# Kernel tuning notes

Measured on AMD Instinct MI355X. Metric: run time of the kernel, lower is better.

## Reference

```python
import math
import jax, jax.numpy as jnp
import numpy as np

B, M, H, K, L = 8, 512, 512, 8, 1024  # batch, block, hidden, heads, span
D = H // K  # head_dim = 64; key/value length = M + L


def _skew(X):
    # shift every row one step right: [B', M, L] -> [B', M, M+L]
    Bp, Mm, Ll = X.shape
    X = jnp.pad(X, ((0, 0), (0, 0), (0, Mm + 1)))
    X = X.reshape(Bp, -1)[:, :-Mm]
    return X.reshape(Bp, Mm, Mm + Ll)


def _unskew(X):
    # reverse of _skew: [B', M, M+L] -> [B', M, L]
    Bp, Mm, Lt = X.shape
    Ll = Lt - Mm
    X = X.reshape(Bp, -1)
    X = jnp.pad(X, ((0, 0), (0, Mm)))
    X = X.reshape(Bp, Mm, Mm + Ll + 1)
    return X[:, :, :Ll]


def _heads(x):
    # [B, T, K*D] -> [B*K, T, D]
    b, t, _ = x.shape
    return x.reshape(b, t, K, D).transpose(0, 2, 1, 3).reshape(b * K, t, D)


def setup_inputs() -> dict:
    key0 = jax.random.key(0)
    ks = jax.random.split(key0, 8)
    s = 1.0 / math.sqrt(H)
    return {
        "query": jax.random.normal(ks[0], (B, M, H), jnp.float32),
        "key": jax.random.normal(ks[1], (B, M + L, H), jnp.float32),
        "value": jax.random.normal(ks[2], (B, M + L, H), jnp.float32),
        "key_pe": jax.random.normal(ks[3], (1, D, L), jnp.float32),
        "Wq": jax.random.normal(ks[4], (H, H), jnp.float32) * s,
        "Wk": jax.random.normal(ks[5], (H, H), jnp.float32) * s,
        "Wv": jax.random.normal(ks[6], (H, H), jnp.float32) * s,
        "Wo": jax.random.normal(ks[7], (H, H), jnp.float32) * s,
    }


def reference(query, key, value, key_pe, Wq, Wk, Wv, Wo):
    q = _heads(query @ Wq.T)   # [B*K, M, D]
    k = _heads(key @ Wk.T)     # [B*K, M+L, D]
    v = _heads(value @ Wv.T)   # [B*K, M+L, D]

    attn_cont = jnp.einsum('bmd,bnd->bmn', q, k)       # [B*K, M, M+L]
    attn_cont = _unskew(attn_cont)                      # [B*K, M, L]
    attn_pos = jnp.einsum('bmd,dl->bml', q, key_pe[0])  # [B*K, M, L]
    attn = jax.nn.softmax((attn_cont + attn_pos) / math.sqrt(D), axis=-1)

    attn_sk = _skew(attn)                               # [B*K, M, M+L]
    out = jnp.einsum('bmn,bnd->bmd', attn_sk, v)        # [B*K, M, D]
    out = out.reshape(B, K, M, D).transpose(0, 2, 1, 3).reshape(B, M, K * D)
    return out @ Wo.T
```

## Files before the change

kernel.cpp:

```cpp
#include <hip/hip_runtime.h>
#include <hip/hip_bf16.h>
#include <cstddef>
#include <math.h>


#define HDIM 512
#define MQ 512
#define NK 1536
#define LSPAN 1024
#define SHIFT 5.0f

typedef _Float16 f16_t;
typedef f16_t f16x8 __attribute__((ext_vector_type(8)));
typedef f16_t f16x4 __attribute__((ext_vector_type(4)));
typedef float f32x4 __attribute__((ext_vector_type(4)));

#define MFMA16F(a, b, c) __builtin_amdgcn_mfma_f32_16x16x32_f16((a), (b), (c), 0, 0, 0)

__device__ __forceinline__ void async_cp16(const void* g, void* l) {
  __builtin_amdgcn_global_load_lds((const __attribute__((address_space(1))) void*)g,
                                   (__attribute__((address_space(3))) void*)l, 16, 0, 0);
}

__global__ void prep_all(const float* __restrict__ q, const float* __restrict__ k,
                         const float* __restrict__ v,
                         const float* __restrict__ Wq, const float* __restrict__ Wk,
                         const float* __restrict__ Wv, const float* __restrict__ Wo,
                         const float* __restrict__ pe,
                         f16_t* __restrict__ q16, f16_t* __restrict__ k16,
                         f16_t* __restrict__ v16,
                         f16_t* __restrict__ wq, f16_t* __restrict__ wk,
                         f16_t* __restrict__ wv, f16_t* __restrict__ wo,
                         f16_t* __restrict__ pet) {
  int y = blockIdx.y;
  int i = blockIdx.x * 256 + threadIdx.x;
  if (y < 3) {
    const float* s = (y == 0) ? q : (y == 1) ? k : v;
    f16_t* d = (y == 0) ? q16 : (y == 1) ? k16 : v16;
    int n4 = (y == 0) ? 524288 : 1572864;
    if (i >= n4) return;
    float4 x = ((const float4*)s)[i];
    f16x4 o;
    o[0] = (f16_t)x.x; o[1] = (f16_t)x.y; o[2] = (f16_t)x.z; o[3] = (f16_t)x.w;
    ((f16x4*)d)[i] = o;
  } else {
    if (i < 262144) {
      int seg = i >> 16, j = i & 65535;
      const float* s = (seg == 0) ? Wq : (seg == 1) ? Wk : (seg == 2) ? Wv : Wo;
      f16_t* d = (seg == 0) ? wq : (seg == 1) ? wk : (seg == 2) ? wv : wo;
      float4 x = ((const float4*)s)[j];
      f16x4 o;
      o[0] = (f16_t)x.x; o[1] = (f16_t)x.y; o[2] = (f16_t)x.z; o[3] = (f16_t)x.w;
      ((f16x4*)d)[j] = o;
    } else if (i < 327680) {
      int j = i - 262144;
      pet[(j & 1023) * 64 + (j >> 10)] = (f16_t)pe[j];
    }
  }
}

__global__ __launch_bounds__(256) void gemm3(
    const f16_t* __restrict__ q16, const f16_t* __restrict__ k16, const f16_t* __restrict__ v16,
    const f16_t* __restrict__ wq, const f16_t* __restrict__ wk, const f16_t* __restrict__ wv,
    f16_t* __restrict__ qo, f16_t* __restrict__ ko, f16_t* __restrict__ vT) {
  __shared__ alignas(16) f16_t As[2][8192];
  __shared__ alignas(16) f16_t Bs[2][8192];

  const int bx = blockIdx.x;
  const f16_t *A, *Bm;
  f16_t* C;
  int row0, col0, ldc;
  if (bx < 128) {
    int t = bx;
    A = q16; Bm = wq; C = qo; ldc = HDIM;
    row0 = (t >> 2) * 128; col0 = (t & 3) * 128;
  } else if (bx < 512) {
    int t = bx - 128;
    A = k16; Bm = wk; C = ko; ldc = HDIM;
    row0 = (t >> 2) * 128; col0 = (t & 3) * 128;
  } else {
    int t = bx - 512;
    int b = t / 48, u = t % 48;
    A = wv; Bm = v16 + (size_t)b * NK * HDIM;
    C = vT + (size_t)b * 512 * NK; ldc = NK;
    row0 = (u / 12) * 128; col0 = (u % 12) * 128;
  }

  const int tid = threadIdx.x;
  const int lane = tid & 63, wave = tid >> 6;
  const int quad = lane >> 4, l16 = lane & 15;
  const int wr = (wave & 1) * 64, wc = (wave >> 1) * 64;
  const int rstage = tid >> 3, cstage = tid & 7;

#pragma unroll
  for (int i = 0; i < 4; ++i) {
    int r = i * 32 + rstage;
    int csw = cstage ^ (r & 7);
    async_cp16(A  + (size_t)(row0 + r) * HDIM + csw * 8, &As[0][i * 2048 + wave * 512]);
    async_cp16(Bm + (size_t)(col0 + r) * HDIM + csw * 8, &Bs[0][i * 2048 + wave * 512]);
  }

  f32x4 acc[4][4] = {};
  for (int it = 0; it < 8; ++it) {
    const int buf = it & 1;
    __syncthreads();
    if (it + 1 < 8) {
      int k0 = (it + 1) * 64;
#pragma unroll
      for (int i = 0; i < 4; ++i) {
        int r = i * 32 + rstage;
        int csw = cstage ^ (r & 7);
        async_cp16(A  + (size_t)(row0 + r) * HDIM + k0 + csw * 8,
                   &As[buf ^ 1][i * 2048 + wave * 512]);
        async_cp16(Bm + (size_t)(col0 + r) * HDIM + k0 + csw * 8,
                   &Bs[buf ^ 1][i * 2048 + wave * 512]);
      }
    }
#pragma unroll
    for (int ks = 0; ks < 2; ++ks) {
      f16x8 af[4], bf[4];
#pragma unroll
      for (int i = 0; i < 4; ++i) {
        int rA = wr + i * 16 + l16;
        af[i] = *(const f16x8*)&As[buf][rA * 64 + (((ks * 4 + quad) ^ (rA & 7)) * 8)];
        int rB = wc + i * 16 + l16;
        bf[i] = *(const f16x8*)&Bs[buf][rB * 64 + (((ks * 4 + quad) ^ (rB & 7)) * 8)];
      }
#pragma unroll
      for (int i = 0; i < 4; ++i)
#pragma unroll
        for (int n = 0; n < 4; ++n)
          acc[i][n] = MFMA16F(af[i], bf[n], acc[i][n]);
    }
  }
#pragma unroll
  for (int i = 0; i < 4; ++i)
#pragma unroll
    for (int n = 0; n < 4; ++n)
#pragma unroll
      for (int r = 0; r < 4; ++r)
        C[(size_t)(row0 + wr + i * 16 + quad * 4 + r) * ldc + col0 + wc + n * 16 + l16] =
            (f16_t)acc[i][n][r];
}

__global__ __launch_bounds__(256) void attn2(const f16_t* __restrict__ q,
                                             const f16_t* __restrict__ k,
                                             const f16_t* __restrict__ vT,
                                             const f16_t* __restrict__ pet,
                                             f16_t* __restrict__ Opart,
                                             float* __restrict__ Lpart) {
  __shared__ alignas(16) f16_t Ks[2][4096];
  __shared__ alignas(16) f16_t Vs[4096];
  __shared__ alignas(16) f16_t Tst[4][128][20];
  __shared__ alignas(16) f16_t Ps[4][16][72];

  const int m0 = blockIdx.x * 64;
  const int bh = blockIdx.y;
  const int b = bh >> 3, kh = bh & 7;
  const int z = blockIdx.z;
  const int j0 = z ? 9 : 0, j1 = z ? 16 : 8;
  const int tid = threadIdx.x;
  const int lane = tid & 63, wave = tid >> 6;
  const int quad = lane >> 4, l16 = lane & 15;
  const int sr = wave * 16;
  const int rstage = tid >> 3, cstage = tid & 7;

  f16_t (*Tw)[20] = Tst[wave];
  f16_t (*Pw)[72] = Ps[wave];

  f16x8 qa0, qa1;
  {
    const f16_t* qrow = q + (size_t)(b * MQ + m0 + sr + l16) * HDIM + kh * 64;
    qa0 = *(const f16x8*)(qrow + quad * 8);
    qa1 = *(const f16x8*)(qrow + 32 + quad * 8);
#pragma unroll
    for (int e = 0; e < 8; ++e) {
      qa0[e] = (f16_t)((float)qa0[e] * 0.125f);
      qa1[e] = (f16_t)((float)qa1[e] * 0.125f);
    }
  }

  f16x8 ones;
#pragma unroll
  for (int e = 0; e < 8; ++e) ones[e] = (f16_t)1.0f;

  f32x4 oacc[4] = {};
  f32x4 lacc = {};

  const f16_t* kbh = k + (size_t)b * NK * HDIM + kh * 64;
  const f16_t* vbh = vT + (size_t)(b * 512 + kh * 64) * NK;

  if (z) {
#pragma unroll
    for (int ch = 0; ch < 4; ++ch) {
      int l = 512 + ch * 16 + l16;
      f16x8 s0 = *(const f16x8*)(pet + (size_t)l * 64 + quad * 8);
      f16x8 s1 = *(const f16x8*)(pet + (size_t)l * 64 + 32 + quad * 8);
      f32x4 tt = {};
      tt = MFMA16F(qa0, s0, tt);
      tt = MFMA16F(qa1, s1, tt);
      int sb = l + sr + quad * 4;
#pragma unroll
      for (int r = 0; r < 4; ++r)
        Tw[(sb + r) & 127][quad * 4 + r] = (f16_t)tt[r];
    }
  }

#pragma unroll
  for (int i = 0; i < 2; ++i) {
    int r = i * 32 + rstage;
    int nsrc = m0 + j0 * 64 + r;
    int csw = cstage ^ (r & 7);
    async_cp16(kbh + (size_t)nsrc * HDIM + csw * 8, &Ks[0][i * 2048 + wave * 512]);
  }

  int buf = 0;
  for (int j = j0; j <= j1; ++j, buf ^= 1) {
    __syncthreads();

    f16x8 pb0[4], pb1[4];
    if (j < 16) {
#pragma unroll
      for (int ch = 0; ch < 4; ++ch) {
        int l = j * 64 + ch * 16 + l16;
        pb0[ch] = *(const f16x8*)(pet + (size_t)l * 64 + quad * 8);
        pb1[ch] = *(const f16x8*)(pet + (size_t)l * 64 + 32 + quad * 8);
      }
    }
    {
      int ncol0 = m0 + j * 64;
#pragma unroll
      for (int i = 0; i < 2; ++i) {
        int d = i * 32 + rstage;
        int csw = cstage ^ (d & 7);
        async_cp16(vbh + (size_t)d * NK + ncol0 + csw * 8, &Vs[i * 2048 + wave * 512]);
      }
#pragma unroll
      for (int i = 0; i < 2; ++i) {
        int r = i * 32 + rstage;
        int nsrc = m0 + (j + 1) * 64 + r;
        nsrc = (nsrc < NK) ? nsrc : (NK - 1);
        int csw = cstage ^ (r & 7);
        async_cp16(kbh + (size_t)nsrc * HDIM + csw * 8, &Ks[buf ^ 1][i * 2048 + wave * 512]);
      }
    }
    if (j < 16) {
      const int l0 = j * 64;
#pragma unroll
      for (int ch = 0; ch < 4; ++ch) {
        f32x4 tt = {};
        tt = MFMA16F(qa0, pb0[ch], tt);
        tt = MFMA16F(qa1, pb1[ch], tt);
        int sb = l0 + ch * 16 + l16 + sr + quad * 4;
#pragma unroll
        for (int r = 0; r < 4; ++r)
          Tw[(sb + r) & 127][quad * 4 + r] = (f16_t)tt[r];
      }
    }
    f32x4 sacc[4];
#pragma unroll
    for (int ch = 0; ch < 4; ++ch) {
      int n = ch * 16 + l16;
      const f16_t* kr = &Ks[buf][n * 64];
      f16x8 kb0 = *(const f16x8*)&kr[(quad ^ (n & 7)) * 8];
      f16x8 kb1 = *(const f16x8*)&kr[((quad + 4) ^ (n & 7)) * 8];
      f32x4 s = {};
      s = MFMA16F(qa0, kb0, s);
      s = MFMA16F(qa1, kb1, s);
      sacc[ch] = s;
    }
#pragma unroll
    for (int ch = 0; ch < 4; ++ch) {
      int scol = (j * 64 + ch * 16 + l16) & 127;
      f16x4 tq = *(const f16x4*)&Tw[scol][quad * 4];
#pragma unroll
      for (int r = 0; r < 4; ++r) {
        int il = quad * 4 + r;
        int l = j * 64 + ch * 16 + l16 - sr - il;
        float pe_ = __expf(sacc[ch][r] + (float)tq[r] - SHIFT);
        float pv = (l >= 0 && l < LSPAN) ? pe_ : 0.f;
        Pw[il][ch * 16 + l16] = (f16_t)pv;
      }
    }
    f16x8 pa0 = *(const f16x8*)&Pw[l16][quad * 8];
    f16x8 pa1 = *(const f16x8*)&Pw[l16][32 + quad * 8];
    __builtin_amdgcn_s_waitcnt(0x0F72);
#pragma unroll
    for (int dch = 0; dch < 4; ++dch) {
      int d = dch * 16 + l16;
      const f16_t* vr = &Vs[d * 64];
      f16x8 vb0 = *(const f16x8*)&vr[(quad ^ (d & 7)) * 8];
      f16x8 vb1 = *(const f16x8*)&vr[((quad + 4) ^ (d & 7)) * 8];
      oacc[dch] = MFMA16F(pa0, vb0, oacc[dch]);
      oacc[dch] = MFMA16F(pa1, vb1, oacc[dch]);
    }
    lacc = MFMA16F(pa0, ones, lacc);
    lacc = MFMA16F(pa1, ones, lacc);
  }

  f16_t* Op = Opart + (size_t)z * 2097152;
#pragma unroll
  for (int r = 0; r < 4; ++r) {
    float inv = 1.0f / lacc[r];
    int m = m0 + sr + quad * 4 + r;
#pragma unroll
    for (int dch = 0; dch < 4; ++dch)
      Op[(size_t)(b * MQ + m) * HDIM + kh * 64 + dch * 16 + l16] =
          (f16_t)(oacc[dch][r] * inv);
    if (l16 == 0)
      Lpart[z * 32768 + bh * MQ + m] = lacc[r];
  }
}

__global__ __launch_bounds__(256) void gemm_wo(const f16_t* __restrict__ O0,
                                               const f16_t* __restrict__ O1,
                                               const float* __restrict__ Lpart,
                                               const f16_t* __restrict__ Bw,
                                               float* __restrict__ C) {
  __shared__ alignas(16) f16_t As[2][128][72];
  __shared__ alignas(16) f16_t Bs[2][4096];
  const int bx = blockIdx.x;
  const int row0 = (bx >> 3) * 128, col0 = (bx & 7) * 64;
  const int tid = threadIdx.x;
  const int lane = tid & 63, wave = tid >> 6;
  const int quad = lane >> 4, l16 = lane & 15;
  const int wr = (wave & 1) * 64, wc = (wave >> 1) * 32;
  const int rstage = tid >> 3, cstage = tid & 7;
  const int cA8 = (tid & 7) * 8;

  f16x8 areg[4];
  auto loadA = [&](int it) {
    int k0 = it * 64;
    int head = (k0 + cA8) >> 6;
#pragma unroll
    for (int i = 0; i < 4; ++i) {
      int rg = row0 + i * 32 + rstage;
      int li = ((rg >> 9) * 8 + head) * MQ + (rg & 511);
      float l0 = Lpart[li], l1 = Lpart[32768 + li];
      float w0 = l0 / (l0 + l1), w1 = 1.0f - w0;
      f16x8 o0 = *(const f16x8*)(O0 + (size_t)rg * HDIM + k0 + cA8);
      f16x8 o1 = *(const f16x8*)(O1 + (size_t)rg * HDIM + k0 + cA8);
      f16x8 a8;
#pragma unroll
      for (int e = 0; e < 8; ++e)
        a8[e] = (f16_t)((float)o0[e] * w0 + (float)o1[e] * w1);
      areg[i] = a8;
    }
  };

  loadA(0);
#pragma unroll
  for (int i = 0; i < 2; ++i) {
    int r = i * 32 + rstage;
    int csw = cstage ^ (r & 7);
    async_cp16(Bw + (size_t)(col0 + r) * HDIM + csw * 8, &Bs[0][i * 2048 + wave * 512]);
  }
#pragma unroll
  for (int i = 0; i < 4; ++i)
    *(f16x8*)&As[0][i * 32 + rstage][cA8] = areg[i];

  f32x4 acc[4][2] = {};
  for (int it = 0; it < 8; ++it) {
    const int buf = it & 1;
    __syncthreads();
    if (it + 1 < 8) {
      int k0 = (it + 1) * 64;
#pragma unroll
      for (int i = 0; i < 2; ++i) {
        int r = i * 32 + rstage;
        int csw = cstage ^ (r & 7);
        async_cp16(Bw + (size_t)(col0 + r) * HDIM + k0 + csw * 8,
                   &Bs[buf ^ 1][i * 2048 + wave * 512]);
      }
      loadA(it + 1);
    }
#pragma unroll
    for (int ks = 0; ks < 2; ++ks) {
      f16x8 af[4], bf[2];
#pragma unroll
      for (int i = 0; i < 4; ++i)
        af[i] = *(const f16x8*)&As[buf][wr + i * 16 + l16][(ks * 4 + quad) * 8];
#pragma unroll
      for (int n = 0; n < 2; ++n) {
        int rB = wc + n * 16 + l16;
        bf[n] = *(const f16x8*)&Bs[buf][rB * 64 + (((ks * 4 + quad) ^ (rB & 7)) * 8)];
      }
#pragma unroll
      for (int i = 0; i < 4; ++i)
#pragma unroll
        for (int n = 0; n < 2; ++n)
          acc[i][n] = MFMA16F(af[i], bf[n], acc[i][n]);
    }
    if (it + 1 < 8) {
#pragma unroll
      for (int i = 0; i < 4; ++i)
        *(f16x8*)&As[buf ^ 1][i * 32 + rstage][cA8] = areg[i];
    }
  }
#pragma unroll
  for (int i = 0; i < 4; ++i)
#pragma unroll
    for (int n = 0; n < 2; ++n)
#pragma unroll
      for (int r = 0; r < 4; ++r)
        C[(size_t)(row0 + wr + i * 16 + quad * 4 + r) * HDIM + col0 + wc + n * 16 + l16] =
            acc[i][n][r];
}

extern "C" void kernel_launch(void* const* d_in, const int* in_sizes, int n_in,
                              void* d_out, int out_size, void* d_ws, size_t ws_size,
                              hipStream_t stream) {
  const float* query  = (const float*)d_in[0];
  const float* key    = (const float*)d_in[1];
  const float* value  = (const float*)d_in[2];
  const float* key_pe = (const float*)d_in[3];
  const float* Wq     = (const float*)d_in[4];
  const float* Wk     = (const float*)d_in[5];
  const float* Wv     = (const float*)d_in[6];
  const float* Wo     = (const float*)d_in[7];
  float* out = (float*)d_out;

  f16_t* ws = (f16_t*)d_ws;
  f16_t* q16a = ws;
  f16_t* k16a = q16a + 2097152;
  f16_t* v16a = k16a + 6291456;
  f16_t* wq16 = v16a + 6291456;
  f16_t* wk16 = wq16 + 262144;
  f16_t* wv16 = wk16 + 262144;
  f16_t* wo16 = wv16 + 262144;
  f16_t* pet  = wo16 + 262144;
  f16_t* qo   = pet + 65536;
  f16_t* ko   = qo + 2097152;
  f16_t* vTo  = ko + 6291456;
  f16_t* Opart = k16a;
  float* Lpart = (float*)v16a;

  hipLaunchKernelGGL(prep_all, dim3(6144, 4), dim3(256), 0, stream,
                     query, key, value, Wq, Wk, Wv, Wo, key_pe,
                     q16a, k16a, v16a, wq16, wk16, wv16, wo16, pet);
  hipLaunchKernelGGL(gemm3, dim3(896), dim3(256), 0, stream,
                     q16a, k16a, v16a, wq16, wk16, wv16, qo, ko, vTo);
  hipLaunchKernelGGL(attn2, dim3(8, 64, 2), dim3(256), 0, stream,
                     qo, ko, vTo, pet, Opart, Lpart);
  hipLaunchKernelGGL(gemm_wo, dim3(256), dim3(256), 0, stream,
                     Opart, Opart + 2097152, Lpart, wo16, out);
}
```

Before: 210.2 us.

## Fold log2e into Q scale, use exp2, skip masking on interior tiles, add setprio

Folds log2(e)/sqrt(D) into the query prescale and the softmax shift into the stored positional term, so the inner loop uses exp2f directly without extra adds. The l-range masking is now applied only on the first and last tiles, since interior tiles never need it. The positional MFMA is moved after the QK MFMAs, s_setprio hints are placed around the MFMA sections, and the positional staging row pitch shrinks from 20 to 18 halves. Together these cut VALU work in the softmax step, at the cost of possible LDS bank conflicts from the new pitch and fp16 rounding of the shifted positional values.

```diff
diff --git a/kernel.cpp b/kernel.cpp
--- a/kernel.cpp
+++ b/kernel.cpp
@@ -8,7 +8,8 @@
 #define MQ 512
 #define NK 1536
 #define LSPAN 1024
-#define SHIFT 5.0f
+#define QSCALE 0.18033688f
+#define SHIFT2 7.2134752f
 
 typedef _Float16 f16_t;
 typedef f16_t f16x8 __attribute__((ext_vector_type(8)));
@@ -151,7 +152,7 @@
                                              float* __restrict__ Lpart) {
   __shared__ alignas(16) f16_t Ks[2][4096];
   __shared__ alignas(16) f16_t Vs[4096];
-  __shared__ alignas(16) f16_t Tst[4][128][20];
+  __shared__ alignas(16) f16_t Tst[4][128][18];
   __shared__ alignas(16) f16_t Ps[4][16][72];
 
   const int m0 = blockIdx.x * 64;
@@ -165,7 +166,7 @@
   const int sr = wave * 16;
   const int rstage = tid >> 3, cstage = tid & 7;
 
-  f16_t (*Tw)[20] = Tst[wave];
+  f16_t (*Tw)[18] = Tst[wave];
   f16_t (*Pw)[72] = Ps[wave];
 
   f16x8 qa0, qa1;
@@ -175,8 +176,8 @@
     qa1 = *(const f16x8*)(qrow + 32 + quad * 8);
 #pragma unroll
     for (int e = 0; e < 8; ++e) {
-      qa0[e] = (f16_t)((float)qa0[e] * 0.125f);
-      qa1[e] = (f16_t)((float)qa1[e] * 0.125f);
+      qa0[e] = (f16_t)((float)qa0[e] * QSCALE);
+      qa1[e] = (f16_t)((float)qa1[e] * QSCALE);
     }
   }
 
@@ -191,9 +192,10 @@
   const f16_t* vbh = vT + (size_t)(b * 512 + kh * 64) * NK;
 
   if (z) {
+    const int lb = (j0 - 1) * 64;
 #pragma unroll
     for (int ch = 0; ch < 4; ++ch) {
-      int l = 512 + ch * 16 + l16;
+      int l = lb + ch * 16 + l16;
       f16x8 s0 = *(const f16x8*)(pet + (size_t)l * 64 + quad * 8);
       f16x8 s1 = *(const f16x8*)(pet + (size_t)l * 64 + 32 + quad * 8);
       f32x4 tt = {};
@@ -202,7 +204,7 @@
       int sb = l + sr + quad * 4;
 #pragma unroll
       for (int r = 0; r < 4; ++r)
-        Tw[(sb + r) & 127][quad * 4 + r] = (f16_t)tt[r];
+        Tw[(sb + r) & 127][quad * 4 + r] = (f16_t)(tt[r] - SHIFT2);
     }
   }
 
@@ -244,20 +246,8 @@
         async_cp16(kbh + (size_t)nsrc * HDIM + csw * 8, &Ks[buf ^ 1][i * 2048 + wave * 512]);
       }
     }
-    if (j < 16) {
-      const int l0 = j * 64;
-#pragma unroll
-      for (int ch = 0; ch < 4; ++ch) {
-        f32x4 tt = {};
-        tt = MFMA16F(qa0, pb0[ch], tt);
-        tt = MFMA16F(qa1, pb1[ch], tt);
-        int sb = l0 + ch * 16 + l16 + sr + quad * 4;
-#pragma unroll
-        for (int r = 0; r < 4; ++r)
-          Tw[(sb + r) & 127][quad * 4 + r] = (f16_t)tt[r];
-      }
-    }
     f32x4 sacc[4];
+    __builtin_amdgcn_s_setprio(1);
 #pragma unroll
     for (int ch = 0; ch < 4; ++ch) {
       int n = ch * 16 + l16;
@@ -269,22 +259,48 @@
       s = MFMA16F(qa1, kb1, s);
       sacc[ch] = s;
     }
-#pragma unroll
-    for (int ch = 0; ch < 4; ++ch) {
-      int scol = (j * 64 + ch * 16 + l16) & 127;
-      f16x4 tq = *(const f16x4*)&Tw[scol][quad * 4];
-#pragma unroll
-      for (int r = 0; r < 4; ++r) {
-        int il = quad * 4 + r;
-        int l = j * 64 + ch * 16 + l16 - sr - il;
-        float pe_ = __expf(sacc[ch][r] + (float)tq[r] - SHIFT);
-        float pv = (l >= 0 && l < LSPAN) ? pe_ : 0.f;
-        Pw[il][ch * 16 + l16] = (f16_t)pv;
+    __builtin_amdgcn_s_setprio(0);
+    if (j < 16) {
+      const int l0 = j * 64;
+#pragma unroll
+      for (int ch = 0; ch < 4; ++ch) {
+        f32x4 tt = {};
+        tt = MFMA16F(qa0, pb0[ch], tt);
+        tt = MFMA16F(qa1, pb1[ch], tt);
+        int sb = l0 + ch * 16 + l16 + sr + quad * 4;
+#pragma unroll
+        for (int r = 0; r < 4; ++r)
+          Tw[(sb + r) & 127][quad * 4 + r] = (f16_t)(tt[r] - SHIFT2);
+      }
+    }
+    if (j != 0 && j != 16) {
+#pragma unroll
+      for (int ch = 0; ch < 4; ++ch) {
+        int scol = (j * 64 + ch * 16 + l16) & 127;
+        f16x4 tq = *(const f16x4*)&Tw[scol][quad * 4];
+#pragma unroll
+        for (int r = 0; r < 4; ++r)
+          Pw[quad * 4 + r][ch * 16 + l16] =
+              (f16_t)exp2f(sacc[ch][r] + (float)tq[r]);
+      }
+    } else {
+#pragma unroll
+      for (int ch = 0; ch < 4; ++ch) {
+        int scol = (j * 64 + ch * 16 + l16) & 127;
+        f16x4 tq = *(const f16x4*)&Tw[scol][quad * 4];
+#pragma unroll
+        for (int r = 0; r < 4; ++r) {
+          int il = quad * 4 + r;
+          int l = j * 64 + ch * 16 + l16 - sr - il;
+          float pe_ = exp2f(sacc[ch][r] + (float)tq[r]);
+          Pw[il][ch * 16 + l16] = (f16_t)((l >= 0 && l < LSPAN) ? pe_ : 0.f);
+        }
       }
     }
     f16x8 pa0 = *(const f16x8*)&Pw[l16][quad * 8];
     f16x8 pa1 = *(const f16x8*)&Pw[l16][32 + quad * 8];
     __builtin_amdgcn_s_waitcnt(0x0F72);
+    __builtin_amdgcn_s_setprio(1);
 #pragma unroll
     for (int dch = 0; dch < 4; ++dch) {
       int d = dch * 16 + l16;
@@ -296,6 +312,7 @@
     }
     lacc = MFMA16F(pa0, ones, lacc);
     lacc = MFMA16F(pa1, ones, lacc);
+    __builtin_amdgcn_s_setprio(0);
   }
 
   f16_t* Op = Opart + (size_t)z * 2097152;
```

After: 219.2 us. 4.3% more time.

## Load K and V fragments directly from global memory instead of LDS staging

Applied to the files above, without the earlier changes.

The attention kernel drops the shared-memory double buffer for K and the V tile, along with the async global-to-LDS copies, the per-iteration __syncthreads and the waitcnt. Each wave now reads its K and V MFMA fragments straight from global memory into registers, and the kernel adds a launch-bounds occupancy hint. The goal is to remove block-wide barriers and LDS traffic so that more waves fit per CU. In exchange, every wave in a block re-reads the same K/V rows from global memory (4x redundant loads through cache), and global load latency is no longer hidden by prefetching.

```diff
diff --git a/kernel.cpp b/kernel.cpp
--- a/kernel.cpp
+++ b/kernel.cpp
@@ -143,14 +143,12 @@
             (f16_t)acc[i][n][r];
 }
 
-__global__ __launch_bounds__(256) void attn2(const f16_t* __restrict__ q,
-                                             const f16_t* __restrict__ k,
-                                             const f16_t* __restrict__ vT,
-                                             const f16_t* __restrict__ pet,
-                                             f16_t* __restrict__ Opart,
-                                             float* __restrict__ Lpart) {
-  __shared__ alignas(16) f16_t Ks[2][4096];
-  __shared__ alignas(16) f16_t Vs[4096];
+__global__ __launch_bounds__(256, 3) void attn2(const f16_t* __restrict__ q,
+                                                const f16_t* __restrict__ k,
+                                                const f16_t* __restrict__ vT,
+                                                const f16_t* __restrict__ pet,
+                                                f16_t* __restrict__ Opart,
+                                                float* __restrict__ Lpart) {
   __shared__ alignas(16) f16_t Tst[4][128][20];
   __shared__ alignas(16) f16_t Ps[4][16][72];
 
@@ -163,7 +161,6 @@
   const int lane = tid & 63, wave = tid >> 6;
   const int quad = lane >> 4, l16 = lane & 15;
   const int sr = wave * 16;
-  const int rstage = tid >> 3, cstage = tid & 7;
 
   f16_t (*Tw)[20] = Tst[wave];
   f16_t (*Pw)[72] = Ps[wave];
@@ -191,9 +188,10 @@
   const f16_t* vbh = vT + (size_t)(b * 512 + kh * 64) * NK;
 
   if (z) {
+    const int lb = (j0 - 1) * 64;
 #pragma unroll
     for (int ch = 0; ch < 4; ++ch) {
-      int l = 512 + ch * 16 + l16;
+      int l = lb + ch * 16 + l16;
       f16x8 s0 = *(const f16x8*)(pet + (size_t)l * 64 + quad * 8);
       f16x8 s1 = *(const f16x8*)(pet + (size_t)l * 64 + 32 + quad * 8);
       f32x4 tt = {};
@@ -206,17 +204,8 @@
     }
   }
 
-#pragma unroll
-  for (int i = 0; i < 2; ++i) {
-    int r = i * 32 + rstage;
-    int nsrc = m0 + j0 * 64 + r;
-    int csw = cstage ^ (r & 7);
-    async_cp16(kbh + (size_t)nsrc * HDIM + csw * 8, &Ks[0][i * 2048 + wave * 512]);
-  }
-
-  int buf = 0;
-  for (int j = j0; j <= j1; ++j, buf ^= 1) {
-    __syncthreads();
+  for (int j = j0; j <= j1; ++j) {
+    const int nrow0 = m0 + j * 64;
 
     f16x8 pb0[4], pb1[4];
     if (j < 16) {
@@ -227,22 +216,12 @@
         pb1[ch] = *(const f16x8*)(pet + (size_t)l * 64 + 32 + quad * 8);
       }
     }
-    {
-      int ncol0 = m0 + j * 64;
-#pragma unroll
-      for (int i = 0; i < 2; ++i) {
-        int d = i * 32 + rstage;
-        int csw = cstage ^ (d & 7);
-        async_cp16(vbh + (size_t)d * NK + ncol0 + csw * 8, &Vs[i * 2048 + wave * 512]);
-      }
-#pragma unroll
-      for (int i = 0; i < 2; ++i) {
-        int r = i * 32 + rstage;
-        int nsrc = m0 + (j + 1) * 64 + r;
-        nsrc = (nsrc < NK) ? nsrc : (NK - 1);
-        int csw = cstage ^ (r & 7);
-        async_cp16(kbh + (size_t)nsrc * HDIM + csw * 8, &Ks[buf ^ 1][i * 2048 + wave * 512]);
-      }
+    f16x8 kb0a[4], kb1a[4];
+#pragma unroll
+    for (int ch = 0; ch < 4; ++ch) {
+      const f16_t* kr = kbh + (size_t)(nrow0 + ch * 16 + l16) * HDIM;
+      kb0a[ch] = *(const f16x8*)(kr + quad * 8);
+      kb1a[ch] = *(const f16x8*)(kr + 32 + quad * 8);
     }
     if (j < 16) {
       const int l0 = j * 64;
@@ -260,14 +239,17 @@
     f32x4 sacc[4];
 #pragma unroll
     for (int ch = 0; ch < 4; ++ch) {
-      int n = ch * 16 + l16;
-      const f16_t* kr = &Ks[buf][n * 64];
-      f16x8 kb0 = *(const f16x8*)&kr[(quad ^ (n & 7)) * 8];
-      f16x8 kb1 = *(const f16x8*)&kr[((quad + 4) ^ (n & 7)) * 8];
       f32x4 s = {};
-      s = MFMA16F(qa0, kb0, s);
-      s = MFMA16F(qa1, kb1, s);
+      s = MFMA16F(qa0, kb0a[ch], s);
+      s = MFMA16F(qa1, kb1a[ch], s);
       sacc[ch] = s;
+    }
+    f16x8 vb0a[4], vb1a[4];
+#pragma unroll
+    for (int dch = 0; dch < 4; ++dch) {
+      const f16_t* vr = vbh + (size_t)(dch * 16 + l16) * NK + nrow0;
+      vb0a[dch] = *(const f16x8*)(vr + quad * 8);
+      vb1a[dch] = *(const f16x8*)(vr + 32 + quad * 8);
     }
 #pragma unroll
     for (int ch = 0; ch < 4; ++ch) {
@@ -284,15 +266,10 @@
     }
     f16x8 pa0 = *(const f16x8*)&Pw[l16][quad * 8];
     f16x8 pa1 = *(const f16x8*)&Pw[l16][32 + quad * 8];
-    __builtin_amdgcn_s_waitcnt(0x0F72);
 #pragma unroll
     for (int dch = 0; dch < 4; ++dch) {
-      int d = dch * 16 + l16;
-      const f16_t* vr = &Vs[d * 64];
-      f16x8 vb0 = *(const f16x8*)&vr[(quad ^ (d & 7)) * 8];
-      f16x8 vb1 = *(const f16x8*)&vr[((quad + 4) ^ (d & 7)) * 8];
-      oacc[dch] = MFMA16F(pa0, vb0, oacc[dch]);
-      oacc[dch] = MFMA16F(pa1, vb1, oacc[dch]);
+      oacc[dch] = MFMA16F(pa0, vb0a[dch], oacc[dch]);
+      oacc[dch] = MFMA16F(pa1, vb1a[dch], oacc[dch]);
     }
     lacc = MFMA16F(pa0, ones, lacc);
     lacc = MFMA16F(pa1, ones, lacc);
```

Measured after the change: 252.5 us. 1.2x slower.
